# Optimization experiments

Hardware: AMD Instinct MI355X
Metric: run time of the kernel (lower is better)

Reference implementation:

```python
import jax, jax.numpy as jnp
import numpy as np


def setup_inputs() -> dict:
    key = jax.random.key(0)
    k1, k2 = jax.random.split(key)
    B, T, D, E = 4, 4096, 2048, 64
    x = jax.random.normal(k1, (B, T, D), dtype=jnp.float32)
    # nn.Linear default init ~ U(-1/sqrt(D), 1/sqrt(D)); scaled normal is fine for a numeric baseline
    W = jax.random.normal(k2, (D, E), dtype=jnp.float32) * (1.0 / np.sqrt(D))
    b = jnp.zeros((E,), dtype=jnp.float32)
    return {"x": x, "W": W, "b": b}


TOPK = 2


def reference(x, W, b):
    # logits: (B, T, E)
    logits = jnp.einsum("btd,de->bte", x, W) + b
    probs = jax.nn.softmax(logits, axis=-1)
    topk_vals, topk_idx = jax.lax.top_k(probs, TOPK)
    return topk_idx, topk_vals
```

## Files before the change

### kernel.cpp

```cpp
#include <hip/hip_runtime.h>
#include <math.h>


#define D_DIM 2048
#define E_DIM 64
#define M_DIM 16384
#define RM 32
#define BKC 64
#define NCHW 8
#define XSTR 68

typedef _Float16 half8 __attribute__((ext_vector_type(8)));
typedef float floatx4 __attribute__((ext_vector_type(4)));
typedef unsigned int uint;

__global__ __launch_bounds__(256) void split_w_kernel(
    const float* __restrict__ Wm, _Float16* __restrict__ wsT)
{
    const int tid = threadIdx.x;
    const int n   = tid & 63;
    const int kk0 = tid >> 6;
    const int g   = blockIdx.x;
    #pragma unroll
    for (int r = 0; r < 8; r++) {
        const int kk = kk0 + r * 4;
        const float v = Wm[(size_t)(g * 32 + kk) * E_DIM + n];
        const _Float16 h = (_Float16)v;
        const _Float16 l = (_Float16)((v - (float)h) * 2048.0f);
        const int t = n >> 4, cc = n & 15, qd = kk >> 3, j = kk & 7;
        const size_t base = (size_t)((g * 4 + t) * 2) * 512 + (size_t)(qd * 16 + cc) * 8 + j;
        wsT[base]       = h;
        wsT[base + 512] = l;
    }
}

__global__ __launch_bounds__(256, 2) void router_mfma_kernel(
    const float* __restrict__ x, const _Float16* __restrict__ wsT,
    const float* __restrict__ bias, float* __restrict__ out)
{
    __shared__ uint xbuf[4][2][RM * XSTR];

    const int lane = threadIdx.x & 63;
    const int wave = threadIdx.x >> 6;
    const int c    = lane & 15;
    const int quad = lane >> 4;
    const int r0   = blockIdx.x * RM;
    const int kb   = wave * (D_DIM / 4);

    const float* xg = x + (size_t)(r0 + quad) * D_DIM + kb + c * 4;
    const _Float16* wbase = wsT + (size_t)(wave * 16) * 4096 + lane * 8;

    floatx4 accm[2][4] = {};
    floatx4 accl[2][4] = {};
    float4 xa[8], xb[8];
    half8 wh0[4], wl0[4], wh1[4], wl1[4];

    auto loadx = [&](int n, float4* dst) {
        const int nn = n < NCHW ? n : NCHW - 1;
        #pragma unroll
        for (int i = 0; i < 8; i++)
            dst[i] = *reinterpret_cast<const float4*>(xg + (size_t)i * 4 * D_DIM + nn * BKC);
    };
    auto stage = [&](int buf, const float4* src) {
        uint* dst = &xbuf[wave][buf][0];
        #pragma unroll
        for (int i = 0; i < 8; i++) {
            const int row = i * 4 + quad;
            const float v[4] = {src[i].x, src[i].y, src[i].z, src[i].w};
            uint p[4];
            #pragma unroll
            for (int q = 0; q < 4; q++) {
                const _Float16 h = (_Float16)v[q];
                const _Float16 l = (_Float16)((v[q] - (float)h) * 2048.0f);
                p[q] = (uint)__builtin_bit_cast(unsigned short, h)
                     | ((uint)__builtin_bit_cast(unsigned short, l) << 16);
            }
            *reinterpret_cast<uint4*>(dst + row * XSTR + c * 4) =
                make_uint4(p[0], p[1], p[2], p[3]);
        }
    };
    auto loadW = [&](int u, half8* wh, half8* wl) {
        const int uu = u < 16 ? u : 15;
        const _Float16* p = wbase + (size_t)uu * 4096;
        #pragma unroll
        for (int t = 0; t < 4; t++) {
            wh[t] = *reinterpret_cast<const half8*>(p + t * 1024);
            wl[t] = *reinterpret_cast<const half8*>(p + t * 1024 + 512);
        }
    };
    auto step = [&](int buf, int s, const half8* wh, const half8* wl) {
        #pragma unroll
        for (int tau = 0; tau < 2; tau++) {
            const uint* rp = &xbuf[wave][buf][(tau * 16 + c) * XSTR + s * 32 + quad * 8];
            uint u8[8];
            *reinterpret_cast<uint4*>(u8)     = *reinterpret_cast<const uint4*>(rp);
            *reinterpret_cast<uint4*>(u8 + 4) = *reinterpret_cast<const uint4*>(rp + 4);
            uint hh[4], ll[4];
            #pragma unroll
            for (int q = 0; q < 4; q++) {
                hh[q] = (u8[2 * q] & 0xffffu) | (u8[2 * q + 1] << 16);
                ll[q] = (u8[2 * q] >> 16) | (u8[2 * q + 1] & 0xffff0000u);
            }
            const half8 ah = __builtin_bit_cast(half8, make_uint4(hh[0], hh[1], hh[2], hh[3]));
            const half8 al = __builtin_bit_cast(half8, make_uint4(ll[0], ll[1], ll[2], ll[3]));
            #pragma unroll
            for (int t = 0; t < 4; t++) {
                accm[tau][t] = __builtin_amdgcn_mfma_f32_16x16x32_f16(ah, wh[t], accm[tau][t], 0, 0, 0);
                accl[tau][t] = __builtin_amdgcn_mfma_f32_16x16x32_f16(al, wh[t], accl[tau][t], 0, 0, 0);
                accl[tau][t] = __builtin_amdgcn_mfma_f32_16x16x32_f16(ah, wl[t], accl[tau][t], 0, 0, 0);
            }
        }
    };

    loadx(0, xa);
    loadx(1, xb);
    loadW(0, wh0, wl0);
    stage(0, xa);

    #pragma unroll 1
    for (int n = 0; n < NCHW; n += 2) {
        loadx(n + 2, xa);
        loadW(2 * n + 1, wh1, wl1);
        stage(1, xb);
        step(0, 0, wh0, wl0);
        loadW(2 * n + 2, wh0, wl0);
        step(0, 1, wh1, wl1);
        loadx(n + 3, xb);
        loadW(2 * n + 3, wh1, wl1);
        if (n + 2 < NCHW) stage(0, xa);
        step(1, 0, wh0, wl0);
        loadW(2 * n + 4, wh0, wl0);
        step(1, 1, wh1, wl1);
    }

    __syncthreads();
    float* red = reinterpret_cast<float*>(&xbuf[0][0][0]);
    const float scale = 1.0f / 2048.0f;
    #pragma unroll
    for (int tau = 0; tau < 2; tau++)
        #pragma unroll
        for (int t = 0; t < 4; t++)
            #pragma unroll
            for (int i = 0; i < 4; i++)
                red[(wave * 32 + tau * 16 + quad * 4 + i) * 65 + c + 16 * t] =
                    accm[tau][t][i] + accl[tau][t][i] * scale;
    __syncthreads();

    if (wave >= 2) return;

    float bvt[4];
    #pragma unroll
    for (int t = 0; t < 4; t++) bvt[t] = bias[c + 16 * t];

    #pragma unroll
    for (int i = 0; i < 4; i++) {
        const int row = wave * 16 + quad * 4 + i;
        float lt[4];
        #pragma unroll
        for (int t = 0; t < 4; t++) {
            const int col = c + 16 * t;
            lt[t] = red[(0 * 32 + row) * 65 + col] + red[(1 * 32 + row) * 65 + col]
                  + red[(2 * 32 + row) * 65 + col] + red[(3 * 32 + row) * 65 + col] + bvt[t];
        }
        const float l0 = lt[0], l1 = lt[1], l2 = lt[2], l3 = lt[3];

        float m = fmaxf(fmaxf(l0, l1), fmaxf(l2, l3));
        #pragma unroll
        for (int off = 1; off < 16; off <<= 1)
            m = fmaxf(m, __shfl_xor(m, off, 64));

        const float e0 = expf(l0 - m), e1 = expf(l1 - m);
        const float e2 = expf(l2 - m), e3 = expf(l3 - m);
        float s = e0 + e1 + e2 + e3;
        #pragma unroll
        for (int off = 1; off < 16; off <<= 1)
            s += __shfl_xor(s, off, 64);

        const float p0 = e0 / s, p1 = e1 / s, p2 = e2 / s, p3 = e3 / s;

        const unsigned long long ka =
            ((unsigned long long)__float_as_uint(p0) << 32) | (unsigned long long)(63 - c);
        const unsigned long long kb_ =
            ((unsigned long long)__float_as_uint(p1) << 32) | (unsigned long long)(47 - c);
        const unsigned long long kc_ =
            ((unsigned long long)__float_as_uint(p2) << 32) | (unsigned long long)(31 - c);
        const unsigned long long kd =
            ((unsigned long long)__float_as_uint(p3) << 32) | (unsigned long long)(15 - c);

        unsigned long long hi1 = ka > kb_ ? ka : kb_, lo1 = ka > kb_ ? kb_ : ka;
        unsigned long long hi2 = kc_ > kd ? kc_ : kd, lo2 = kc_ > kd ? kd : kc_;
        unsigned long long k1 = hi1 > hi2 ? hi1 : hi2;
        unsigned long long mn = hi1 > hi2 ? hi2 : hi1;
        unsigned long long mx = lo1 > lo2 ? lo1 : lo2;
        unsigned long long k2 = mn > mx ? mn : mx;

        #pragma unroll
        for (int off = 1; off < 16; off <<= 1) {
            const unsigned long long o1 = __shfl_xor(k1, off, 64);
            const unsigned long long o2 = __shfl_xor(k2, off, 64);
            const unsigned long long n1 = k1 > o1 ? k1 : o1;
            const unsigned long long w1 = k1 > o1 ? o1 : k1;
            const unsigned long long w2 = k2 > o2 ? k2 : o2;
            k1 = n1;
            k2 = w1 > w2 ? w1 : w2;
        }

        if (c == 0) {
            const int gr = r0 + row;
            out[gr * 2 + 0] = (float)(63 - (int)(k1 & 0xFFFFFFFFull));
            out[gr * 2 + 1] = (float)(63 - (int)(k2 & 0xFFFFFFFFull));
            out[M_DIM * 2 + gr * 2 + 0] = __uint_as_float((unsigned)(k1 >> 32));
            out[M_DIM * 2 + gr * 2 + 1] = __uint_as_float((unsigned)(k2 >> 32));
        }
    }
}

extern "C" void kernel_launch(void* const* d_in, const int* in_sizes, int n_in,
                              void* d_out, int out_size, void* d_ws, size_t ws_size,
                              hipStream_t stream) {
    const float* x  = (const float*)d_in[0];
    const float* Wm = (const float*)d_in[1];
    const float* b  = (const float*)d_in[2];
    float* out = (float*)d_out;
    _Float16* wsT = (_Float16*)d_ws;

    split_w_kernel<<<dim3(64), dim3(256), 0, stream>>>(Wm, wsT);
    router_mfma_kernel<<<dim3(M_DIM / RM), dim3(256), 0, stream>>>(x, wsT, b, out);
}
```

Baseline: 202.6 us.

## Split router GEMM across waves by expert tile instead of K range

New measurement: 210.8 us. 4.1% more time.

```diff
diff --git a/kernel.cpp b/kernel.cpp
--- a/kernel.cpp
+++ b/kernel.cpp
@@ -5,9 +5,9 @@
 #define D_DIM 2048
 #define E_DIM 64
 #define M_DIM 16384
-#define RM 32
+#define RM 16
 #define BKC 64
-#define NCHW 8
+#define NCH 32
 #define XSTR 68
 
 typedef _Float16 half8 __attribute__((ext_vector_type(8)));
@@ -34,64 +34,52 @@
     }
 }
 
-__global__ __launch_bounds__(256, 2) void router_mfma_kernel(
+__global__ __launch_bounds__(256, 4) void router_mfma_kernel(
     const float* __restrict__ x, const _Float16* __restrict__ wsT,
     const float* __restrict__ bias, float* __restrict__ out)
 {
-    __shared__ uint xbuf[4][2][RM * XSTR];
-
-    const int lane = threadIdx.x & 63;
-    const int wave = threadIdx.x >> 6;
+    __shared__ uint xbuf[2][RM * XSTR];
+
+    const int tid  = threadIdx.x;
+    const int lane = tid & 63;
+    const int wave = tid >> 6;
     const int c    = lane & 15;
     const int quad = lane >> 4;
+    const int rs   = tid >> 4;
+    const int c4   = tid & 15;
     const int r0   = blockIdx.x * RM;
-    const int kb   = wave * (D_DIM / 4);
-
-    const float* xg = x + (size_t)(r0 + quad) * D_DIM + kb + c * 4;
-    const _Float16* wbase = wsT + (size_t)(wave * 16) * 4096 + lane * 8;
-
-    floatx4 accm[2][4] = {};
-    floatx4 accl[2][4] = {};
-    float4 xa[8], xb[8];
-    half8 wh0[4], wl0[4], wh1[4], wl1[4];
-
-    auto loadx = [&](int n, float4* dst) {
-        const int nn = n < NCHW ? n : NCHW - 1;
-        #pragma unroll
-        for (int i = 0; i < 8; i++)
-            dst[i] = *reinterpret_cast<const float4*>(xg + (size_t)i * 4 * D_DIM + nn * BKC);
-    };
-    auto stage = [&](int buf, const float4* src) {
-        uint* dst = &xbuf[wave][buf][0];
-        #pragma unroll
-        for (int i = 0; i < 8; i++) {
-            const int row = i * 4 + quad;
-            const float v[4] = {src[i].x, src[i].y, src[i].z, src[i].w};
-            uint p[4];
-            #pragma unroll
-            for (int q = 0; q < 4; q++) {
-                const _Float16 h = (_Float16)v[q];
-                const _Float16 l = (_Float16)((v[q] - (float)h) * 2048.0f);
-                p[q] = (uint)__builtin_bit_cast(unsigned short, h)
-                     | ((uint)__builtin_bit_cast(unsigned short, l) << 16);
-            }
-            *reinterpret_cast<uint4*>(dst + row * XSTR + c * 4) =
-                make_uint4(p[0], p[1], p[2], p[3]);
-        }
-    };
-    auto loadW = [&](int u, half8* wh, half8* wl) {
-        const int uu = u < 16 ? u : 15;
-        const _Float16* p = wbase + (size_t)uu * 4096;
-        #pragma unroll
-        for (int t = 0; t < 4; t++) {
-            wh[t] = *reinterpret_cast<const half8*>(p + t * 1024);
-            wl[t] = *reinterpret_cast<const half8*>(p + t * 1024 + 512);
-        }
-    };
-    auto step = [&](int buf, int s, const half8* wh, const half8* wl) {
-        #pragma unroll
-        for (int tau = 0; tau < 2; tau++) {
-            const uint* rp = &xbuf[wave][buf][(tau * 16 + c) * XSTR + s * 32 + quad * 8];
+
+    const float*    xg = x   + (size_t)(r0 + rs) * D_DIM + c4 * 4;
+    const _Float16* wt = wsT + (size_t)wave * 1024 + (size_t)lane * 8;
+
+    floatx4 accm = {0.f, 0.f, 0.f, 0.f};
+    floatx4 accl = {0.f, 0.f, 0.f, 0.f};
+    float4 ra, rb;
+
+    auto xload = [&](int n) -> float4 {
+        const int nn = n < NCH ? n : NCH - 1;
+        return *reinterpret_cast<const float4*>(xg + nn * BKC);
+    };
+    auto stage = [&](int buf, const float4& v4) {
+        const float v[4] = {v4.x, v4.y, v4.z, v4.w};
+        uint p[4];
+        #pragma unroll
+        for (int q = 0; q < 4; q++) {
+            const _Float16 h = (_Float16)v[q];
+            const _Float16 l = (_Float16)((v[q] - (float)h) * 2048.0f);
+            p[q] = (uint)__builtin_bit_cast(unsigned short, h)
+                 | ((uint)__builtin_bit_cast(unsigned short, l) << 16);
+        }
+        *reinterpret_cast<uint4*>(&xbuf[buf][rs * XSTR + c4 * 4]) =
+            make_uint4(p[0], p[1], p[2], p[3]);
+    };
+    auto compute = [&](int buf, int n) {
+        #pragma unroll
+        for (int s = 0; s < 2; s++) {
+            const _Float16* wp = wt + (size_t)(2 * n + s) * 4096;
+            const half8 wh = *reinterpret_cast<const half8*>(wp);
+            const half8 wl = *reinterpret_cast<const half8*>(wp + 512);
+            const uint* rp = &xbuf[buf][c * XSTR + s * 32 + quad * 8];
             uint u8[8];
             *reinterpret_cast<uint4*>(u8)     = *reinterpret_cast<const uint4*>(rp);
             *reinterpret_cast<uint4*>(u8 + 4) = *reinterpret_cast<const uint4*>(rp + 4);
@@ -103,65 +91,55 @@
             }
             const half8 ah = __builtin_bit_cast(half8, make_uint4(hh[0], hh[1], hh[2], hh[3]));
             const half8 al = __builtin_bit_cast(half8, make_uint4(ll[0], ll[1], ll[2], ll[3]));
-            #pragma unroll
-            for (int t = 0; t < 4; t++) {
-                accm[tau][t] = __builtin_amdgcn_mfma_f32_16x16x32_f16(ah, wh[t], accm[tau][t], 0, 0, 0);
-                accl[tau][t] = __builtin_amdgcn_mfma_f32_16x16x32_f16(al, wh[t], accl[tau][t], 0, 0, 0);
-                accl[tau][t] = __builtin_amdgcn_mfma_f32_16x16x32_f16(ah, wl[t], accl[tau][t], 0, 0, 0);
-            }
-        }
-    };
-
-    loadx(0, xa);
-    loadx(1, xb);
-    loadW(0, wh0, wl0);
-    stage(0, xa);
+            accm = __builtin_amdgcn_mfma_f32_16x16x32_f16(ah, wh, accm, 0, 0, 0);
+            accl = __builtin_amdgcn_mfma_f32_16x16x32_f16(al, wh, accl, 0, 0, 0);
+            accl = __builtin_amdgcn_mfma_f32_16x16x32_f16(ah, wl, accl, 0, 0, 0);
+        }
+    };
+    auto barrier_lds = [&]() {
+        asm volatile("s_waitcnt lgkmcnt(0)" ::: "memory");
+        __builtin_amdgcn_s_barrier();
+        asm volatile("" ::: "memory");
+    };
+
+    ra = xload(0);
+    rb = xload(1);
+    stage(0, ra);
+    ra = xload(2);
 
     #pragma unroll 1
-    for (int n = 0; n < NCHW; n += 2) {
-        loadx(n + 2, xa);
-        loadW(2 * n + 1, wh1, wl1);
-        stage(1, xb);
-        step(0, 0, wh0, wl0);
-        loadW(2 * n + 2, wh0, wl0);
-        step(0, 1, wh1, wl1);
-        loadx(n + 3, xb);
-        loadW(2 * n + 3, wh1, wl1);
-        if (n + 2 < NCHW) stage(0, xa);
-        step(1, 0, wh0, wl0);
-        loadW(2 * n + 4, wh0, wl0);
-        step(1, 1, wh1, wl1);
+    for (int n = 0; n < NCH; n += 2) {
+        barrier_lds();
+        compute(0, n);
+        stage(1, rb);
+        rb = xload(n + 3);
+        barrier_lds();
+        compute(1, n + 1);
+        if (n + 2 < NCH) stage(0, ra);
+        ra = xload(n + 4);
     }
 
     __syncthreads();
-    float* red = reinterpret_cast<float*>(&xbuf[0][0][0]);
+    float* red = reinterpret_cast<float*>(&xbuf[0][0]);
     const float scale = 1.0f / 2048.0f;
     #pragma unroll
-    for (int tau = 0; tau < 2; tau++)
+    for (int i = 0; i < 4; i++)
+        red[(quad * 4 + i) * 65 + wave * 16 + c] = accm[i] + accl[i] * scale;
+    __syncthreads();
+
+    if (wave != 0) return;
+
+    float bvt[4];
+    #pragma unroll
+    for (int t = 0; t < 4; t++) bvt[t] = bias[c + 16 * t];
+
+    #pragma unroll
+    for (int i = 0; i < 4; i++) {
+        const int row = quad * 4 + i;
+        float lt[4];
         #pragma unroll
         for (int t = 0; t < 4; t++)
-            #pragma unroll
-            for (int i = 0; i < 4; i++)
-                red[(wave * 32 + tau * 16 + quad * 4 + i) * 65 + c + 16 * t] =
-                    accm[tau][t][i] + accl[tau][t][i] * scale;
-    __syncthreads();
-
-    if (wave >= 2) return;
-
-    float bvt[4];
-    #pragma unroll
-    for (int t = 0; t < 4; t++) bvt[t] = bias[c + 16 * t];
-
-    #pragma unroll
-    for (int i = 0; i < 4; i++) {
-        const int row = wave * 16 + quad * 4 + i;
-        float lt[4];
-        #pragma unroll
-        for (int t = 0; t < 4; t++) {
-            const int col = c + 16 * t;
-            lt[t] = red[(0 * 32 + row) * 65 + col] + red[(1 * 32 + row) * 65 + col]
-                  + red[(2 * 32 + row) * 65 + col] + red[(3 * 32 + row) * 65 + col] + bvt[t];
-        }
+            lt[t] = red[row * 65 + 16 * t + c] + bvt[t];
         const float l0 = lt[0], l1 = lt[1], l2 = lt[2], l3 = lt[3];
 
         float m = fmaxf(fmaxf(l0, l1), fmaxf(l2, l3));
```
